# Performance work log

Measured on AMD Instinct MI355X. Metric: run time of the kernel, lower is better.

Reference implementation:

```python
import jax, jax.numpy as jnp
import numpy as np

NUM_HEADS = 12
HEAD_DIM = 64
SCALE = HEAD_DIM ** -0.5


def setup_inputs() -> dict:
    key = jax.random.key(0)
    ks = jax.random.split(key, 5)
    B, N, C = 8, 1024, 768
    x = jax.random.normal(ks[0], (B, N, C), dtype=jnp.float32)
    qkv_w = jax.random.normal(ks[1], (3 * C, C), dtype=jnp.float32) * (C ** -0.5)
    qkv_b = jax.random.normal(ks[2], (3 * C,), dtype=jnp.float32) * 0.02
    proj_w = jax.random.normal(ks[3], (C, C), dtype=jnp.float32) * (C ** -0.5)
    proj_b = jax.random.normal(ks[4], (C,), dtype=jnp.float32) * 0.02
    return {"x": x, "qkv_w": qkv_w, "qkv_b": qkv_b, "proj_w": proj_w, "proj_b": proj_b}


def reference(x, qkv_w, qkv_b, proj_w, proj_b):
    B, N, C = x.shape
    H, D = NUM_HEADS, HEAD_DIM
    # qkv projection: (B,N,3C) -> (3,B,H,N,D)
    qkv = (x @ qkv_w.T + qkv_b).reshape(B, N, 3, H, D).transpose(2, 0, 3, 1, 4)
    q, k, v = qkv[0], qkv[1], qkv[2]
    q = q * SCALE
    # full N x N attention scores, softmax over keys
    attn = jax.nn.softmax(jnp.einsum("bhnd,bhmd->bhnm", q, k), axis=-1)
    # Libragrad: detach the softmax map before multiplying with V
    attn = jax.lax.stop_gradient(attn)
    out = jnp.einsum("bhnm,bhmd->bhnd", attn, v)  # (B,H,N,D)
    out = out.transpose(0, 2, 1, 3).reshape(B, N, C)
    return out @ proj_w.T + proj_b
```

## Files before the change

kernel.cpp:

```cpp
#include <hip/hip_runtime.h>

#define NH 12
#define HD 64
#define BB 8
#define SEQ 1024
#define CD 768

typedef __bf16 bf16x8 __attribute__((ext_vector_type(8)));
typedef float f32x4 __attribute__((ext_vector_type(4)));

__device__ __forceinline__ unsigned short f2bf(float f) {
    unsigned int u = __float_as_uint(f);
    u = (u + 0x7fffu + ((u >> 16) & 1u)) >> 16;
    return (unsigned short)u;
}

__device__ __forceinline__ void gld_lds16(const unsigned short* g, unsigned short* l) {
    __builtin_amdgcn_global_load_lds(
        (const __attribute__((address_space(1))) unsigned int*)g,
        (__attribute__((address_space(3))) unsigned int*)l, 16, 0, 0);
}

#define N4_X 1572864
#define N4_W1 442368
#define N4_W2 147456
__global__ void cast_all(const float* __restrict__ x, const float* __restrict__ w1,
                         const float* __restrict__ w2,
                         unsigned short* __restrict__ ox, unsigned short* __restrict__ ow1,
                         unsigned short* __restrict__ ow2) {
    int i = blockIdx.x * blockDim.x + threadIdx.x;
    const float4* src;
    ushort4* dst;
    if (i < N4_X) {
        src = (const float4*)x + i; dst = (ushort4*)ox + i;
    } else if (i < N4_X + N4_W1) {
        src = (const float4*)w1 + (i - N4_X); dst = (ushort4*)ow1 + (i - N4_X);
    } else if (i < N4_X + N4_W1 + N4_W2) {
        src = (const float4*)w2 + (i - N4_X - N4_W1); dst = (ushort4*)ow2 + (i - N4_X - N4_W1);
    } else return;
    float4 f = *src;
    ushort4 o;
    o.x = f2bf(f.x); o.y = f2bf(f.y); o.z = f2bf(f.z); o.w = f2bf(f.w);
    *dst = o;
}

template<int MODE>
__global__ __launch_bounds__(256)
void gemm_bt(const unsigned short* __restrict__ A, const unsigned short* __restrict__ W,
             const float* __restrict__ bias,
             unsigned short* __restrict__ qb, unsigned short* __restrict__ kb,
             unsigned short* __restrict__ vb, float* __restrict__ fout,
             int M, int N, int K) {
    __shared__ __attribute__((aligned(16))) unsigned short As[128 * 32];
    __shared__ __attribute__((aligned(16))) unsigned short Bs[128 * 32];

    const int t    = threadIdx.x;
    const int bm0  = blockIdx.x * 128;
    const int bn0  = blockIdx.y * 128;
    const int wave = t >> 6;
    const int lane = t & 63;
    const int wm   = (wave >> 1) * 64;
    const int wn   = (wave & 1) * 64;
    const int col  = lane & 15;
    const int quad = lane >> 4;

    const int srow = t >> 2;
    const int scol = (t & 3) * 8;

    f32x4 acc[4][4];
#pragma unroll
    for (int i = 0; i < 4; i++)
#pragma unroll
        for (int j = 0; j < 4; j++) acc[i][j] = (f32x4){0.f, 0.f, 0.f, 0.f};

    for (int k0 = 0; k0 < K; k0 += 32) {
        __syncthreads();
        gld_lds16(A + (size_t)(bm0 + srow) * K + k0 + scol,      As + srow * 32 + scol);
        gld_lds16(A + (size_t)(bm0 + 64 + srow) * K + k0 + scol, As + (64 + srow) * 32 + scol);
        gld_lds16(W + (size_t)(bn0 + srow) * K + k0 + scol,      Bs + srow * 32 + scol);
        gld_lds16(W + (size_t)(bn0 + 64 + srow) * K + k0 + scol, Bs + (64 + srow) * 32 + scol);
        __syncthreads();

        bf16x8 af[4], bf[4];
#pragma unroll
        for (int mi = 0; mi < 4; mi++)
            af[mi] = *(const bf16x8*)(As + (wm + mi * 16 + col) * 32 + quad * 8);
#pragma unroll
        for (int ni = 0; ni < 4; ni++)
            bf[ni] = *(const bf16x8*)(Bs + (wn + ni * 16 + col) * 32 + quad * 8);
#pragma unroll
        for (int mi = 0; mi < 4; mi++)
#pragma unroll
            for (int ni = 0; ni < 4; ni++)
                acc[mi][ni] = __builtin_amdgcn_mfma_f32_16x16x32_bf16(
                    af[mi], bf[ni], acc[mi][ni], 0, 0, 0);
    }

    if (MODE == 1) {
#pragma unroll
        for (int mi = 0; mi < 4; mi++)
#pragma unroll
            for (int ni = 0; ni < 4; ni++) {
                const int n = bn0 + wn + ni * 16 + col;
                const float bv = bias[n];
#pragma unroll
                for (int r = 0; r < 4; r++) {
                    const int m = bm0 + wm + mi * 16 + quad * 4 + r;
                    fout[(size_t)m * N + n] = acc[mi][ni][r] + bv;
                }
            }
        return;
    }

    const int sel = bn0 / 768;
    const int nb  = bn0 - sel * 768;
    const int b   = bm0 >> 10;
    const int nqb = bm0 & 1023;
    unsigned short* const dstbuf = (sel == 0) ? qb : (sel == 1) ? kb : vb;
    const float scale = (sel == 0) ? 0.125f : 1.0f;

#pragma unroll
    for (int ni = 0; ni < 4; ni++) {
        const int hn = nb + wn + ni * 16;
        const int h  = hn >> 6;
        const int d0 = hn & 63;
        const float bv = bias[bn0 + wn + ni * 16 + col];
        unsigned short* const rowbase =
            dstbuf + ((size_t)(b * NH + h) * SEQ) * HD + d0 + col;
#pragma unroll
        for (int mi = 0; mi < 4; mi++)
#pragma unroll
            for (int r = 0; r < 4; r++) {
                const int nq = nqb + wm + mi * 16 + quad * 4 + r;
                rowbase[(size_t)nq * HD] = f2bf((acc[mi][ni][r] + bv) * scale);
            }
    }
}

__global__ __launch_bounds__(256, 3)
void attn_mfma(const unsigned short* __restrict__ qb,
               const unsigned short* __restrict__ kb,
               const unsigned short* __restrict__ vb,
               unsigned short* __restrict__ ob) {
    __shared__ __attribute__((aligned(16))) unsigned short Ks[64 * 72];
    __shared__ __attribute__((aligned(16))) unsigned short VT[64 * 72];
    __shared__ __attribute__((aligned(16))) unsigned short Ps[128 * 76];

    const int t  = threadIdx.x;
    const int bh = blockIdx.x;
    const int qt = blockIdx.y;
    const size_t base = (size_t)bh * SEQ * HD;

    const int sr = t >> 2;
    const int sc = (t & 3) * 16;

    const int wave = t >> 6;
    const int lane = t & 63;
    const int col  = lane & 15;
    const int quad = lane >> 4;

    bf16x8 aq[2][2];
#pragma unroll
    for (int u = 0; u < 2; u++) {
        const int q = qt * 128 + (2 * wave + u) * 16 + col;
        aq[u][0] = *(const bf16x8*)(qb + base + (size_t)q * HD + quad * 8);
        aq[u][1] = *(const bf16x8*)(qb + base + (size_t)q * HD + 32 + quad * 8);
    }

    float l_r[2][4];
#pragma unroll
    for (int u = 0; u < 2; u++)
#pragma unroll
        for (int r = 0; r < 4; r++) l_r[u][r] = 0.f;
    f32x4 accO[2][4];
#pragma unroll
    for (int u = 0; u < 2; u++)
#pragma unroll
        for (int di = 0; di < 4; di++) accO[u][di] = (f32x4){0.f, 0.f, 0.f, 0.f};

    const unsigned short* kp = kb + base + (size_t)sr * HD + sc;
    const unsigned short* vp = vb + base + (size_t)sr * HD + sc;
    uint4 kr0 = *(const uint4*)kp,  kr1 = *(const uint4*)(kp + 8);
    uint4 vr0 = *(const uint4*)vp,  vr1 = *(const uint4*)(vp + 8);

    const int vpos = (sr & 15) * 4 + (sr >> 4);

    for (int kc = 0; kc < 16; kc++) {
        __syncthreads();
        *(uint4*)(Ks + sr * 72 + sc)     = kr0;
        *(uint4*)(Ks + sr * 72 + sc + 8) = kr1;
        {
            union { uint4 u4[2]; unsigned short us[16]; } vv;
            vv.u4[0] = vr0; vv.u4[1] = vr1;
#pragma unroll
            for (int j = 0; j < 16; j++)
                VT[(sc + j) * 72 + vpos] = vv.us[j];
        }
        __syncthreads();

        if (kc < 15) {
            const unsigned short* kn = kp + (size_t)(kc + 1) * 64 * HD;
            const unsigned short* vn = vp + (size_t)(kc + 1) * 64 * HD;
            kr0 = *(const uint4*)kn; kr1 = *(const uint4*)(kn + 8);
            vr0 = *(const uint4*)vn; vr1 = *(const uint4*)(vn + 8);
        }

        f32x4 accS[2][4];
#pragma unroll
        for (int ni = 0; ni < 4; ni++) {
            bf16x8 bk0 = *(const bf16x8*)(Ks + (ni * 16 + col) * 72 + quad * 8);
            bf16x8 bk1 = *(const bf16x8*)(Ks + (ni * 16 + col) * 72 + 32 + quad * 8);
#pragma unroll
            for (int u = 0; u < 2; u++) {
                f32x4 z = (f32x4){0.f, 0.f, 0.f, 0.f};
                z = __builtin_amdgcn_mfma_f32_16x16x32_bf16(aq[u][0], bk0, z, 0, 0, 0);
                z = __builtin_amdgcn_mfma_f32_16x16x32_bf16(aq[u][1], bk1, z, 0, 0, 0);
                accS[u][ni] = z;
            }
        }

#pragma unroll
        for (int u = 0; u < 2; u++) {
            const int prow = (2 * wave + u) * 16;
#pragma unroll
            for (int r = 0; r < 4; r++) {
                float p0 = __expf(accS[u][0][r]);
                float p1 = __expf(accS[u][1][r]);
                float p2 = __expf(accS[u][2][r]);
                float p3 = __expf(accS[u][3][r]);
                l_r[u][r] += (p0 + p1) + (p2 + p3);
                uint2 pk;
                pk.x = ((unsigned)f2bf(p1) << 16) | f2bf(p0);
                pk.y = ((unsigned)f2bf(p3) << 16) | f2bf(p2);
                *(uint2*)(Ps + (prow + quad * 4 + r) * 76 + col * 4) = pk;
            }
        }

        bf16x8 ap[2][2];
#pragma unroll
        for (int u = 0; u < 2; u++) {
            const int prow = (2 * wave + u) * 16;
            ap[u][0] = *(const bf16x8*)(Ps + (prow + col) * 76 + quad * 8);
            ap[u][1] = *(const bf16x8*)(Ps + (prow + col) * 76 + 32 + quad * 8);
        }
#pragma unroll
        for (int di = 0; di < 4; di++) {
            bf16x8 bv0 = *(const bf16x8*)(VT + (di * 16 + col) * 72 + quad * 8);
            bf16x8 bv1 = *(const bf16x8*)(VT + (di * 16 + col) * 72 + 32 + quad * 8);
#pragma unroll
            for (int u = 0; u < 2; u++) {
                accO[u][di] = __builtin_amdgcn_mfma_f32_16x16x32_bf16(ap[u][0], bv0, accO[u][di], 0, 0, 0);
                accO[u][di] = __builtin_amdgcn_mfma_f32_16x16x32_bf16(ap[u][1], bv1, accO[u][di], 0, 0, 0);
            }
        }
    }

    const int b = bh / NH, h = bh - b * NH;
#pragma unroll
    for (int u = 0; u < 2; u++)
#pragma unroll
        for (int r = 0; r < 4; r++) {
            float s = l_r[u][r];
            s += __shfl_xor(s, 1);
            s += __shfl_xor(s, 2);
            s += __shfl_xor(s, 4);
            s += __shfl_xor(s, 8);
            const float inv = 1.f / s;
            const int q = qt * 128 + (2 * wave + u) * 16 + quad * 4 + r;
            const size_t rowbase = ((size_t)b * SEQ + q) * CD + h * 64;
#pragma unroll
            for (int di = 0; di < 4; di++)
                ob[rowbase + di * 16 + col] = f2bf(accO[u][di][r] * inv);
        }
}

extern "C" void kernel_launch(void* const* d_in, const int* in_sizes, int n_in,
                              void* d_out, int out_size, void* d_ws, size_t ws_size,
                              hipStream_t stream) {
    const float* x      = (const float*)d_in[0];
    const float* qkv_w  = (const float*)d_in[1];
    const float* qkv_b  = (const float*)d_in[2];
    const float* proj_w = (const float*)d_in[3];
    const float* proj_b = (const float*)d_in[4];
    float* out = (float*)d_out;

    char* ws = (char*)d_ws;
    unsigned short* x_bf     = (unsigned short*)ws;
    unsigned short* attn_bf  = x_bf;
    unsigned short* qkvw_bf  = (unsigned short*)(ws + 12582912);
    unsigned short* projw_bf = (unsigned short*)(ws + 12582912 + 3538944);
    unsigned short* q_bf     = (unsigned short*)(ws + 12582912 + 3538944 + 1179648);
    unsigned short* k_bf     = q_bf + 6291456;
    unsigned short* v_bf     = k_bf + 6291456;

    cast_all<<<8448, 256, 0, stream>>>(x, qkv_w, proj_w, x_bf, qkvw_bf, projw_bf);

    gemm_bt<0><<<dim3(64, 18), 256, 0, stream>>>(x_bf, qkvw_bf, qkv_b,
                                                 q_bf, k_bf, v_bf, nullptr,
                                                 8192, 2304, 768);

    attn_mfma<<<dim3(96, 8), 256, 0, stream>>>(q_bf, k_bf, v_bf, attn_bf);

    gemm_bt<1><<<dim3(64, 6), 256, 0, stream>>>(attn_bf, projw_bf, proj_b,
                                                nullptr, nullptr, nullptr, out,
                                                8192, 768, 768);
}
```

Before: 203.3 us.

## Store V pre-transposed from QKV GEMM and transpose the score MFMA layout

The QKV projection epilogue now writes V directly in a head-dim-major (transposed) layout with vectorized 4-wide stores. This lets the attention kernel copy V tiles into shared memory with 16-byte stores instead of a 16-element scalar scatter transpose. The score MFMA swaps its operands so each lane holds a column of probabilities, which allows packed bf16 stores of P and collapses the row-sum reduction to two cross-quad shuffles. Q is prescaled by log2(e)/sqrt(d) so exp2 replaces __expf. Softmax still uses no max subtraction, so overflow risk is unchanged, and the bf16 conversion switches to the compiler cast.

```diff
diff --git a/kernel.cpp b/kernel.cpp
--- a/kernel.cpp
+++ b/kernel.cpp
@@ -116,8 +116,31 @@
     const int nb  = bn0 - sel * 768;
     const int b   = bm0 >> 10;
     const int nqb = bm0 & 1023;
-    unsigned short* const dstbuf = (sel == 0) ? qb : (sel == 1) ? kb : vb;
-    const float scale = (sel == 0) ? 0.125f : 1.0f;
+
+    if (sel == 2) {
+#pragma unroll
+        for (int ni = 0; ni < 4; ni++) {
+            const int hn = nb + wn + ni * 16;
+            const int h  = hn >> 6;
+            const int d0 = hn & 63;
+            const float bv = bias[bn0 + wn + ni * 16 + col];
+            unsigned short* const rowb =
+                vb + ((size_t)(b * NH + h) * HD + d0 + col) * SEQ + nqb + wm;
+#pragma unroll
+            for (int mi = 0; mi < 4; mi++) {
+                ushort4 o;
+                o.x = f2bf(acc[mi][ni][0] + bv);
+                o.y = f2bf(acc[mi][ni][1] + bv);
+                o.z = f2bf(acc[mi][ni][2] + bv);
+                o.w = f2bf(acc[mi][ni][3] + bv);
+                *(ushort4*)(rowb + mi * 16 + quad * 4) = o;
+            }
+        }
+        return;
+    }
+
+    unsigned short* const dstbuf = (sel == 0) ? qb : kb;
+    const float scale = (sel == 0) ? 0.18033688f : 1.0f;
 
 #pragma unroll
     for (int ni = 0; ni < 4; ni++) {
@@ -167,45 +190,34 @@
         aq[u][1] = *(const bf16x8*)(qb + base + (size_t)q * HD + 32 + quad * 8);
     }
 
-    float l_r[2][4];
+    float l_r[2] = {0.f, 0.f};
+    f32x4 accO[2][4];
 #pragma unroll
     for (int u = 0; u < 2; u++)
 #pragma unroll
-        for (int r = 0; r < 4; r++) l_r[u][r] = 0.f;
-    f32x4 accO[2][4];
-#pragma unroll
-    for (int u = 0; u < 2; u++)
-#pragma unroll
         for (int di = 0; di < 4; di++) accO[u][di] = (f32x4){0.f, 0.f, 0.f, 0.f};
 
     const unsigned short* kp = kb + base + (size_t)sr * HD + sc;
-    const unsigned short* vp = vb + base + (size_t)sr * HD + sc;
+    const unsigned short* vp = vb + base + (size_t)sr * SEQ + sc;
     uint4 kr0 = *(const uint4*)kp,  kr1 = *(const uint4*)(kp + 8);
     uint4 vr0 = *(const uint4*)vp,  vr1 = *(const uint4*)(vp + 8);
-
-    const int vpos = (sr & 15) * 4 + (sr >> 4);
 
     for (int kc = 0; kc < 16; kc++) {
         __syncthreads();
         *(uint4*)(Ks + sr * 72 + sc)     = kr0;
         *(uint4*)(Ks + sr * 72 + sc + 8) = kr1;
-        {
-            union { uint4 u4[2]; unsigned short us[16]; } vv;
-            vv.u4[0] = vr0; vv.u4[1] = vr1;
-#pragma unroll
-            for (int j = 0; j < 16; j++)
-                VT[(sc + j) * 72 + vpos] = vv.us[j];
-        }
+        *(uint4*)(VT + sr * 72 + sc)     = vr0;
+        *(uint4*)(VT + sr * 72 + sc + 8) = vr1;
         __syncthreads();
 
         if (kc < 15) {
             const unsigned short* kn = kp + (size_t)(kc + 1) * 64 * HD;
-            const unsigned short* vn = vp + (size_t)(kc + 1) * 64 * HD;
+            const unsigned short* vn = vp + (size_t)(kc + 1) * 64;
             kr0 = *(const uint4*)kn; kr1 = *(const uint4*)(kn + 8);
             vr0 = *(const uint4*)vn; vr1 = *(const uint4*)(vn + 8);
         }
 
-        f32x4 accS[2][4];
+        f32x4 accT[2][4];
 #pragma unroll
         for (int ni = 0; ni < 4; ni++) {
             bf16x8 bk0 = *(const bf16x8*)(Ks + (ni * 16 + col) * 72 + quad * 8);
@@ -213,9 +225,9 @@
 #pragma unroll
             for (int u = 0; u < 2; u++) {
                 f32x4 z = (f32x4){0.f, 0.f, 0.f, 0.f};
-                z = __builtin_amdgcn_mfma_f32_16x16x32_bf16(aq[u][0], bk0, z, 0, 0, 0);
-                z = __builtin_amdgcn_mfma_f32_16x16x32_bf16(aq[u][1], bk1, z, 0, 0, 0);
-                accS[u][ni] = z;
+                z = __builtin_amdgcn_mfma_f32_16x16x32_bf16(bk0, aq[u][0], z, 0, 0, 0);
+                z = __builtin_amdgcn_mfma_f32_16x16x32_bf16(bk1, aq[u][1], z, 0, 0, 0);
+                accT[u][ni] = z;
             }
         }
 
@@ -223,16 +235,16 @@
         for (int u = 0; u < 2; u++) {
             const int prow = (2 * wave + u) * 16;
 #pragma unroll
-            for (int r = 0; r < 4; r++) {
-                float p0 = __expf(accS[u][0][r]);
-                float p1 = __expf(accS[u][1][r]);
-                float p2 = __expf(accS[u][2][r]);
-                float p3 = __expf(accS[u][3][r]);
-                l_r[u][r] += (p0 + p1) + (p2 + p3);
-                uint2 pk;
-                pk.x = ((unsigned)f2bf(p1) << 16) | f2bf(p0);
-                pk.y = ((unsigned)f2bf(p3) << 16) | f2bf(p2);
-                *(uint2*)(Ps + (prow + quad * 4 + r) * 76 + col * 4) = pk;
+            for (int ni = 0; ni < 4; ni++) {
+                float p0 = __builtin_exp2f(accT[u][ni][0]);
+                float p1 = __builtin_exp2f(accT[u][ni][1]);
+                float p2 = __builtin_exp2f(accT[u][ni][2]);
+                float p3 = __builtin_exp2f(accT[u][ni][3]);
+                l_r[u] += (p0 + p1) + (p2 + p3);
+                union { __bf16 b[4]; uint2 u2; } pk;
+                pk.b[0] = (__bf16)p0; pk.b[1] = (__bf16)p1;
+                pk.b[2] = (__bf16)p2; pk.b[3] = (__bf16)p3;
+                *(uint2*)(Ps + (prow + col) * 76 + ni * 16 + quad * 4) = pk.u2;
             }
         }
 
@@ -257,21 +269,20 @@
 
     const int b = bh / NH, h = bh - b * NH;
 #pragma unroll
-    for (int u = 0; u < 2; u++)
+    for (int u = 0; u < 2; u++) {
+        float s = l_r[u];
+        s += __shfl_xor(s, 16);
+        s += __shfl_xor(s, 32);
 #pragma unroll
         for (int r = 0; r < 4; r++) {
-            float s = l_r[u][r];
-            s += __shfl_xor(s, 1);
-            s += __shfl_xor(s, 2);
-            s += __shfl_xor(s, 4);
-            s += __shfl_xor(s, 8);
-            const float inv = 1.f / s;
+            const float inv = 1.f / __shfl(s, quad * 4 + r);
             const int q = qt * 128 + (2 * wave + u) * 16 + quad * 4 + r;
             const size_t rowbase = ((size_t)b * SEQ + q) * CD + h * 64;
 #pragma unroll
             for (int di = 0; di < 4; di++)
                 ob[rowbase + di * 16 + col] = f2bf(accO[u][di][r] * inv);
         }
+    }
 }
 
 extern "C" void kernel_launch(void* const* d_in, const int* in_sizes, int n_in,
```

Measured after the change: 212.8 us. 1.05x slower.
